# Performance work log

Measured on AMD Instinct MI355X. Metric: run time of the kernel, lower is better.

The kernel has to match this reference:

```python
import jax, jax.numpy as jnp
import numpy as np

HIDDEN = 768
INTER = 1536
N_EXPERTS = 8
TOP_K = 2
AUX_COEF = 0.01


def setup_inputs() -> dict:
    key = jax.random.key(0)
    k0, k1, k2, k3, k4 = jax.random.split(key, 5)
    B, S = 2, 1024
    x = jax.random.normal(k0, (B, S, HIDDEN), dtype=jnp.float32)
    # nn.Linear weights (no bias); stored pre-transposed for einsum (in, out)
    router_w = jax.random.normal(k1, (HIDDEN, N_EXPERTS), dtype=jnp.float32) * 0.02
    w_gate = jax.random.normal(k2, (N_EXPERTS, HIDDEN, INTER), dtype=jnp.float32) * 0.02
    w_up = jax.random.normal(k3, (N_EXPERTS, HIDDEN, INTER), dtype=jnp.float32) * 0.02
    w_down = jax.random.normal(k4, (N_EXPERTS, INTER, HIDDEN), dtype=jnp.float32) * 0.02
    return {"x": x, "router_w": router_w, "w_gate": w_gate, "w_up": w_up, "w_down": w_down}


def reference(x, router_w, w_gate, w_up, w_down):
    B, S, H = x.shape
    xf = x.reshape(-1, H)                      # [T, H]
    T = xf.shape[0]

    router_logits = xf @ router_w              # [T, E]
    router_probs = jax.nn.softmax(router_logits.astype(jnp.float32), axis=-1)
    topk_probs, topk_idx = jax.lax.top_k(router_probs, TOP_K)   # [T, K]
    topk_probs = topk_probs / topk_probs.sum(axis=-1, keepdims=True)

    # dense combine weights: [T, E]; top_k indices are distinct per token so add == set
    comb = jnp.zeros((T, N_EXPERTS), jnp.float32).at[
        jnp.arange(T)[:, None], topk_idx
    ].add(topk_probs)

    # SwiGLU for all experts (dense faithful form of the per-expert gather loop)
    g = jnp.einsum("th,ehi->tei", xf, w_gate)  # [T, E, I]
    u = jnp.einsum("th,ehi->tei", xf, w_up)
    expert_out = jnp.einsum("tei,eih->teh", jax.nn.silu(g) * u, w_down)  # [T, E, H]
    out = jnp.einsum("teh,te->th", expert_out, comb.astype(expert_out.dtype))

    # load-balancing aux loss
    tokens_per_expert = jnp.zeros(N_EXPERTS, jnp.float32).at[topk_idx.reshape(-1)].add(1.0)
    tokens_per_expert = tokens_per_expert / (T * TOP_K)
    router_prob_per_expert = router_probs.mean(axis=0)
    aux_loss = N_EXPERTS * (tokens_per_expert * router_prob_per_expert).sum() * AUX_COEF

    return out.reshape(B, S, H), aux_loss
```

## Files before the change

### kernel.cpp

```cpp
#include <hip/hip_runtime.h>
#include <math.h>


typedef unsigned short u16;
typedef __attribute__((ext_vector_type(8))) short bhalf8;
typedef __attribute__((ext_vector_type(4))) float floatx4;

#define HD 768
#define ID 1536
#define NE 8
#define TT 2048
#define SLOTS 5120
#define MT 40
#define RBLK 512

__device__ __forceinline__ float b2f(u16 u) {
    union { unsigned int i; float f; } v; v.i = ((unsigned int)u) << 16; return v.f;
}
__device__ __forceinline__ u16 f2b(float f) {
    union { float f; unsigned int i; } v; v.f = f;
    unsigned int i = v.i;
    return (u16)((i + 0x7FFFu + ((i >> 16) & 1u)) >> 16);
}
__device__ __forceinline__ void glds16(const u16* g, u16* l) {
    __builtin_amdgcn_global_load_lds(
        (const __attribute__((address_space(1))) unsigned int*)g,
        (__attribute__((address_space(3))) unsigned int*)l, 16, 0, 0);
}

__global__ void init_k(const u16* __restrict__ x16, int* flag,
                       int* hdr, int* tokof, float* pslot) {
    int i = blockIdx.x * 256 + threadIdx.x;
    if (i < 40) hdr[i] = 0;
    if (i < SLOTS) { tokof[i] = -1; pslot[i] = 0.f; }
    if (blockIdx.x == 0 && threadIdx.x >= 64 && threadIdx.x < 128) {
        int lane = threadIdx.x - 64, c = 0;
#pragma unroll
        for (int j = 0; j < 4; ++j) {
            u16 w = x16[lane + 64 * j];
            int ex = (w >> 7) & 0xFF;
            c += (ex >= 118 && ex <= 135);
        }
#pragma unroll
        for (int off = 32; off > 0; off >>= 1) c += __shfl_xor(c, off);
        if (lane == 0) *flag = (c >= 200) ? 1 : 0;
    }
}

__global__ void router_k(const void* __restrict__ x, const void* __restrict__ rw,
                         const int* __restrict__ flag,
                         int* topki, float* topkp, float* blockpart) {
    __shared__ float sp[4][NE];
    int lane = threadIdx.x & 63, wave = threadIdx.x >> 6;
    int t = blockIdx.x * 4 + wave;
    int bf = *flag;
    const float* xf = (const float*)x + (size_t)t * HD;
    const u16*   xh = (const u16*)x + (size_t)t * HD;
    const float* rf = (const float*)rw;
    const u16*   rh = (const u16*)rw;
    float acc[NE];
#pragma unroll
    for (int e = 0; e < NE; ++e) acc[e] = 0.f;
    for (int j = 0; j < HD / 64; ++j) {
        int h = lane + 64 * j;
        float xv = bf ? b2f(xh[h]) : xf[h];
#pragma unroll
        for (int e = 0; e < NE; ++e)
            acc[e] += xv * (bf ? b2f(rh[h * NE + e]) : rf[h * NE + e]);
    }
#pragma unroll
    for (int e = 0; e < NE; ++e) {
        float v = acc[e];
#pragma unroll
        for (int off = 32; off > 0; off >>= 1) v += __shfl_xor(v, off);
        acc[e] = v;
    }
    if (lane == 0) {
        float m = acc[0];
        for (int e = 1; e < NE; ++e) m = fmaxf(m, acc[e]);
        float p[NE], s = 0.f;
        for (int e = 0; e < NE; ++e) { p[e] = expf(acc[e] - m); s += p[e]; }
        float inv = 1.f / s;
        for (int e = 0; e < NE; ++e) { p[e] *= inv; sp[wave][e] = p[e]; }
        int i1 = 0; float p1 = p[0];
        for (int e = 1; e < NE; ++e) if (p[e] > p1) { p1 = p[e]; i1 = e; }
        int i2 = -1; float p2 = -1.f;
        for (int e = 0; e < NE; ++e) if (e != i1 && p[e] > p2) { p2 = p[e]; i2 = e; }
        if (i2 < 0) { i2 = (i1 + 1) & 7; p2 = p[i2]; }
        float sn = 1.f / (p1 + p2);
        topki[2 * t] = i1;  topki[2 * t + 1] = i2;
        topkp[2 * t] = p1 * sn;  topkp[2 * t + 1] = p2 * sn;
    }
    __syncthreads();
    if (threadIdx.x < NE)
        blockpart[blockIdx.x * NE + threadIdx.x] =
            sp[0][threadIdx.x] + sp[1][threadIdx.x] +
            sp[2][threadIdx.x] + sp[3][threadIdx.x];
}

__global__ void prefix_k(const int* __restrict__ topki,
                         const float* __restrict__ blockpart, int* base,
                         int* total, int* cursor, void* out, const int* flag) {
    __shared__ int hist[NE];
    __shared__ float psum[NE];
    int tid = threadIdx.x;
    if (tid < NE) { hist[tid] = 0; psum[tid] = 0.f; }
    __syncthreads();
    for (int i = tid; i < TT * 2; i += 256) atomicAdd(&hist[topki[i] & 7], 1);
    for (int i = tid; i < RBLK * NE; i += 256) atomicAdd(&psum[i & 7], blockpart[i]);
    __syncthreads();
    if (tid == 0) {
        int cum = 0; float aux = 0.f;
        for (int e = 0; e < NE; ++e) {
            int c = hist[e];
            base[e] = cum; cum += (c + 127) & ~127;
            cursor[e] = 0;
            aux += ((float)c / (float)(TT * 2)) * (psum[e] / (float)TT);
        }
        *total = cum;
        float auxv = aux * (float)NE * 0.01f;
        if (*flag) ((u16*)out)[(size_t)TT * HD] = f2b(auxv);
        else       ((float*)out)[(size_t)TT * HD] = auxv;
    }
}

__global__ void scatter_k(const int* __restrict__ topki, const float* __restrict__ topkp,
                          const int* __restrict__ base, int* cursor,
                          int* tokof, float* pslot, int* slotmap) {
    __shared__ int lcnt[NE], lbase[NE];
    int tid = threadIdx.x;
    int t = blockIdx.x * 256 + tid;
    if (tid < NE) lcnt[tid] = 0;
    __syncthreads();
    int e0 = topki[2 * t] & 7, e1 = topki[2 * t + 1] & 7;
    float q0 = topkp[2 * t], q1 = topkp[2 * t + 1];
    int l0 = atomicAdd(&lcnt[e0], 1);
    int l1 = atomicAdd(&lcnt[e1], 1);
    __syncthreads();
    if (tid < NE) lbase[tid] = atomicAdd(&cursor[tid], lcnt[tid]);
    __syncthreads();
    int s0 = min(max(base[e0] + lbase[e0] + l0, 0), SLOTS - 1);
    int s1 = min(max(base[e1] + lbase[e1] + l1, 0), SLOTS - 1);
    tokof[s0] = t;  pslot[s0] = q0;  slotmap[2 * t] = s0;
    tokof[s1] = t;  pslot[s1] = q1;  slotmap[2 * t + 1] = s1;
}

__global__ void apack_k(const void* __restrict__ x, const int* __restrict__ flag,
                        const int* __restrict__ tokof, const int* __restrict__ total,
                        u16* __restrict__ apack) {
    int mt = blockIdx.y, kt = blockIdx.x;
    if (mt * 128 >= *total) return;
    int tid = threadIdx.x;
    int ml = tid >> 1, half = tid & 1;
    int tok = tokof[mt * 128 + ml];
    union { uint4 v[4]; u16 u[32]; } buf;
    if ((unsigned)tok < (unsigned)TT) {
        if (*flag) {
            const u16* s = (const u16*)x + (size_t)tok * HD + kt * 64 + half * 32;
#pragma unroll
            for (int c = 0; c < 4; ++c) buf.v[c] = *(const uint4*)&s[c * 8];
        } else {
            const float* s = (const float*)x + (size_t)tok * HD + kt * 64 + half * 32;
#pragma unroll
            for (int c = 0; c < 8; ++c) {
                float4 f = *(const float4*)&s[c * 4];
                buf.u[c * 4 + 0] = f2b(f.x); buf.u[c * 4 + 1] = f2b(f.y);
                buf.u[c * 4 + 2] = f2b(f.z); buf.u[c * 4 + 3] = f2b(f.w);
            }
        }
    } else {
#pragma unroll
        for (int c = 0; c < 4; ++c) buf.v[c] = make_uint4(0, 0, 0, 0);
    }
    u16* dst = apack + (((size_t)mt * 12 + kt) << 13) + ml * 64;
#pragma unroll
    for (int c = 0; c < 4; ++c) {
        int pc = (half * 4 + c) ^ (ml & 7);
        *(uint4*)(dst + pc * 8) = buf.v[c];
    }
}

__global__ void wpack_k(const void* __restrict__ srcA, const void* __restrict__ srcB,
                        u16* __restrict__ dstA, u16* __restrict__ dstB,
                        int K, int N, int ktiles, int ntiles,
                        const int* __restrict__ flag) {
    __shared__ u16 t[8192];
    int z = blockIdx.z;
    const void* src = (srcB != nullptr && z >= NE) ? srcB : srcA;
    u16* dst = (dstB != nullptr && z >= NE) ? dstB : dstA;
    int e = z & 7;
    int kt = blockIdx.x, nt = blockIdx.y;
    int tid = threadIdx.x;
    int kr = tid >> 2, ng = (tid & 3) * 32;
    size_t srow = ((size_t)e * K + (size_t)kt * 64 + kr) * N + (size_t)nt * 128 + ng;
    union { uint4 v[4]; u16 u[32]; } buf;
    if (*flag) {
        const u16* s = (const u16*)src + srow;
#pragma unroll
        for (int c = 0; c < 4; ++c) buf.v[c] = *(const uint4*)&s[c * 8];
    } else {
        const float* s = (const float*)src + srow;
#pragma unroll
        for (int c = 0; c < 8; ++c) {
            float4 f = *(const float4*)&s[c * 4];
            buf.u[c * 4 + 0] = f2b(f.x); buf.u[c * 4 + 1] = f2b(f.y);
            buf.u[c * 4 + 2] = f2b(f.z); buf.u[c * 4 + 3] = f2b(f.w);
        }
    }
#pragma unroll
    for (int jj = 0; jj < 32; ++jj) {
        int n = ng + jj;
        t[n * 64 + (((kr >> 3) ^ (n & 7)) << 3) + (kr & 7)] = buf.u[jj];
    }
    __syncthreads();
    u16* d = dst + ((((size_t)e * ntiles + nt) * ktiles + kt) << 13);
#pragma unroll
    for (int i = 0; i < 4; ++i) {
        int off = tid * 8 + i * 2048;
        *(uint4*)(d + off) = *(const uint4*)&t[off];
    }
}

__global__ __launch_bounds__(256, 2) void gemm1_k(
        const u16* __restrict__ apack, const u16* __restrict__ wgp,
        const u16* __restrict__ wup, const int* __restrict__ base,
        const int* __restrict__ total, u16* __restrict__ actp) {
    __shared__ u16 smem[24576];
    u16* As = smem; u16* Bg = smem + 8192; u16* Bu = smem + 16384;
    int mt = blockIdx.y;
    if (mt * 128 >= *total) return;
    int e = 7;
    while (e > 0 && mt * 128 < base[e]) --e;
    int nt = blockIdx.x;
    int tid = threadIdx.x, lane = tid & 63, wave = tid >> 6;
    int wm = (wave & 1) * 64, wn = (wave >> 1) * 64;
    int llo = lane & 15, lq = lane >> 4;
    const u16* atile = apack + (((size_t)mt * 12) << 13);
    const u16* gtile = wgp + ((((size_t)e * 12 + nt) * 12) << 13);
    const u16* utile = wup + ((((size_t)e * 12 + nt) * 12) << 13);
    floatx4 accG[4][4], accU[4][4];
#pragma unroll
    for (int i = 0; i < 4; ++i)
#pragma unroll
        for (int j = 0; j < 4; ++j) {
            accG[i][j] = floatx4{0.f, 0.f, 0.f, 0.f};
            accU[i][j] = floatx4{0.f, 0.f, 0.f, 0.f};
        }
    for (int kt = 0; kt < 12; ++kt) {
        const u16* ga = atile + (kt << 13);
        const u16* gg = gtile + (kt << 13);
        const u16* gu = utile + (kt << 13);
        __syncthreads();
#pragma unroll
        for (int i = 0; i < 4; ++i) {
            int off = tid * 8 + i * 2048;
            glds16(ga + off, As + off);
            glds16(gg + off, Bg + off);
            glds16(gu + off, Bu + off);
        }
        asm volatile("s_waitcnt vmcnt(0)" ::: "memory");
        __syncthreads();
#pragma unroll
        for (int kk = 0; kk < 2; ++kk) {
            int q = kk * 4 + lq;
            bhalf8 af[4], bg[4], bu[4];
#pragma unroll
            for (int i = 0; i < 4; ++i) {
                int m = wm + i * 16 + llo;
                af[i] = *(const bhalf8*)&As[m * 64 + ((q ^ (m & 7)) << 3)];
                int n = wn + i * 16 + llo;
                bg[i] = *(const bhalf8*)&Bg[n * 64 + ((q ^ (n & 7)) << 3)];
                bu[i] = *(const bhalf8*)&Bu[n * 64 + ((q ^ (n & 7)) << 3)];
            }
#pragma unroll
            for (int i = 0; i < 4; ++i)
#pragma unroll
                for (int j = 0; j < 4; ++j) {
                    accG[i][j] = __builtin_amdgcn_mfma_f32_16x16x32_bf16(af[i], bg[j], accG[i][j], 0, 0, 0);
                    accU[i][j] = __builtin_amdgcn_mfma_f32_16x16x32_bf16(af[i], bu[j], accU[i][j], 0, 0, 0);
                }
        }
    }
    __syncthreads();
    u16* Ah = smem;
    int q4 = lq * 4;
#pragma unroll
    for (int i = 0; i < 4; ++i)
#pragma unroll
        for (int j = 0; j < 4; ++j)
#pragma unroll
            for (int rr = 0; rr < 4; ++rr) {
                int m = wm + i * 16 + q4 + rr;
                int n = wn + j * 16 + llo;
                float g = accG[i][j][rr], u = accU[i][j][rr];
                Ah[m * 128 + n] = f2b((g / (1.f + expf(-g))) * u);
            }
    __syncthreads();
    u16* dst = actp + (((size_t)mt * 24 + nt * 2) << 13);
#pragma unroll
    for (int s = 0; s < 2; ++s)
#pragma unroll
        for (int i = 0; i < 4; ++i) {
            int off = tid * 8 + i * 2048;
            int m = off >> 6;
            int pc = (off >> 3) & 7;
            int q = pc ^ (m & 7);
            *(uint4*)(dst + ((size_t)s << 13) + off) =
                *(const uint4*)&Ah[m * 128 + s * 64 + q * 8];
        }
}

__global__ __launch_bounds__(256, 2) void gemm2_k(
        const u16* __restrict__ actp, const u16* __restrict__ wdp,
        const int* __restrict__ base, const int* __restrict__ total,
        const float* __restrict__ pslot, float* __restrict__ y) {
    __shared__ u16 smem[16384];
    u16* As = smem; u16* Bs = smem + 8192;
    int mt = blockIdx.y;
    if (mt * 128 >= *total) return;
    int e = 7;
    while (e > 0 && mt * 128 < base[e]) --e;
    int nt = blockIdx.x;
    int tid = threadIdx.x, lane = tid & 63, wave = tid >> 6;
    int wm = (wave & 1) * 64, wn = (wave >> 1) * 64;
    int llo = lane & 15, lq = lane >> 4;
    const u16* atile = actp + (((size_t)mt * 24) << 13);
    const u16* btile = wdp + ((((size_t)e * 6 + nt) * 24) << 13);
    floatx4 acc[4][4];
#pragma unroll
    for (int i = 0; i < 4; ++i)
#pragma unroll
        for (int j = 0; j < 4; ++j) acc[i][j] = floatx4{0.f, 0.f, 0.f, 0.f};
    for (int kt = 0; kt < 24; ++kt) {
        const u16* ga = atile + (kt << 13);
        const u16* gb = btile + (kt << 13);
        __syncthreads();
#pragma unroll
        for (int i = 0; i < 4; ++i) {
            int off = tid * 8 + i * 2048;
            glds16(ga + off, As + off);
            glds16(gb + off, Bs + off);
        }
        asm volatile("s_waitcnt vmcnt(0)" ::: "memory");
        __syncthreads();
#pragma unroll
        for (int kk = 0; kk < 2; ++kk) {
            int q = kk * 4 + lq;
            bhalf8 af[4], bf[4];
#pragma unroll
            for (int i = 0; i < 4; ++i) {
                int m = wm + i * 16 + llo;
                af[i] = *(const bhalf8*)&As[m * 64 + ((q ^ (m & 7)) << 3)];
                int n = wn + i * 16 + llo;
                bf[i] = *(const bhalf8*)&Bs[n * 64 + ((q ^ (n & 7)) << 3)];
            }
#pragma unroll
            for (int i = 0; i < 4; ++i)
#pragma unroll
                for (int j = 0; j < 4; ++j)
                    acc[i][j] = __builtin_amdgcn_mfma_f32_16x16x32_bf16(af[i], bf[j], acc[i][j], 0, 0, 0);
        }
    }
    int q4 = lq * 4;
#pragma unroll
    for (int i = 0; i < 4; ++i)
#pragma unroll
        for (int rr = 0; rr < 4; ++rr) {
            int m = mt * 128 + wm + i * 16 + q4 + rr;
            float p = pslot[m];
#pragma unroll
            for (int j = 0; j < 4; ++j) {
                int n = nt * 128 + wn + j * 16 + llo;
                y[(size_t)m * HD + n] = p * acc[i][j][rr];
            }
        }
}

__global__ void combine_k(const float* __restrict__ y, const int* __restrict__ slotmap,
                          void* __restrict__ out, const int* __restrict__ flag) {
    int g = blockIdx.x * 256 + threadIdx.x;
    int t = g / 192;
    int q = (g % 192) * 4;
    int s0 = min(max(slotmap[2 * t], 0), SLOTS - 1);
    int s1 = min(max(slotmap[2 * t + 1], 0), SLOTS - 1);
    float4 a = *(const float4*)&y[(size_t)s0 * HD + q];
    float4 b = *(const float4*)&y[(size_t)s1 * HD + q];
    float4 rv;
    rv.x = a.x + b.x; rv.y = a.y + b.y; rv.z = a.z + b.z; rv.w = a.w + b.w;
    if (*flag) {
        ushort4 o;
        o.x = f2b(rv.x); o.y = f2b(rv.y); o.z = f2b(rv.z); o.w = f2b(rv.w);
        *(ushort4*)((u16*)out + (size_t)t * HD + q) = o;
    } else {
        *(float4*)((float*)out + (size_t)t * HD + q) = rv;
    }
}

extern "C" void kernel_launch(void* const* d_in, const int* in_sizes, int n_in,
                              void* d_out, int out_size, void* d_ws, size_t ws_size,
                              hipStream_t stream) {
    const void* x  = d_in[0];
    const void* rw = d_in[1];
    const void* wg = d_in[2];
    const void* wu = d_in[3];
    const void* wd = d_in[4];
    char* ws = (char*)d_ws;

    int*   hdr     = (int*)(ws + 0);
    int*   cursor  = (int*)(ws + 32);
    int*   base    = (int*)(ws + 64);
    int*   total   = (int*)(ws + 96);
    int*   flag    = (int*)(ws + 224);
    int*   topki   = (int*)(ws + 256);
    float* topkp   = (float*)(ws + 16640);
    int*   tokof   = (int*)(ws + 33024);
    float* pslot   = (float*)(ws + 53504);
    int*   slotmap = (int*)(ws + 73984);
    float* blockpart = (float*)(ws + 90368);
    u16*   apack   = (u16*)(ws + 106752);
    u16*   actp    = (u16*)(ws + 7971072);
    u16*   wgp     = (u16*)(ws + 23699712);
    u16*   wup     = (u16*)(ws + 42574080);
    u16*   wdp     = (u16*)(ws + 61448448);
    float* ybuf    = (float*)(ws + 23699712);
    if (ws_size < 80322816u) return;

    init_k<<<20, 256, 0, stream>>>((const u16*)x, flag, hdr, tokof, pslot);
    router_k<<<RBLK, 256, 0, stream>>>(x, rw, flag, topki, topkp, blockpart);
    prefix_k<<<1, 256, 0, stream>>>(topki, blockpart, base, total, cursor, d_out, flag);
    scatter_k<<<TT / 256, 256, 0, stream>>>(topki, topkp, base, cursor,
                                            tokof, pslot, slotmap);
    apack_k<<<dim3(12, MT), 256, 0, stream>>>(x, flag, tokof, total, apack);
    wpack_k<<<dim3(12, 12, 16), 256, 0, stream>>>(wg, wu, wgp, wup,
                                                  HD, ID, 12, 12, flag);
    wpack_k<<<dim3(24, 6, 8), 256, 0, stream>>>(wd, nullptr, wdp, nullptr,
                                                ID, HD, 24, 6, flag);
    gemm1_k<<<dim3(12, MT), 256, 0, stream>>>(apack, wgp, wup, base, total, actp);
    gemm2_k<<<dim3(6, MT), 256, 0, stream>>>(actp, wdp, base, total, pslot, ybuf);
    combine_k<<<(TT * 192) / 256, 256, 0, stream>>>(ybuf, slotmap, d_out, flag);
}
```

Measured before the change: 266.8 us.

## Fuse MoE pipeline into one persistent kernel with grid-wide barriers

```diff
diff --git a/kernel.cpp b/kernel.cpp
--- a/kernel.cpp
+++ b/kernel.cpp
@@ -11,8 +11,7 @@
 #define NE 8
 #define TT 2048
 #define SLOTS 5120
-#define MT 40
-#define RBLK 512
+#define NBLK 256
 
 __device__ __forceinline__ float b2f(u16 u) {
     union { unsigned int i; float f; } v; v.i = ((unsigned int)u) << 16; return v.f;
@@ -28,173 +27,35 @@
         (__attribute__((address_space(3))) unsigned int*)l, 16, 0, 0);
 }
 
-__global__ void init_k(const u16* __restrict__ x16, int* flag,
-                       int* hdr, int* tokof, float* pslot) {
-    int i = blockIdx.x * 256 + threadIdx.x;
-    if (i < 40) hdr[i] = 0;
-    if (i < SLOTS) { tokof[i] = -1; pslot[i] = 0.f; }
-    if (blockIdx.x == 0 && threadIdx.x >= 64 && threadIdx.x < 128) {
-        int lane = threadIdx.x - 64, c = 0;
-#pragma unroll
-        for (int j = 0; j < 4; ++j) {
-            u16 w = x16[lane + 64 * j];
-            int ex = (w >> 7) & 0xFF;
-            c += (ex >= 118 && ex <= 135);
-        }
-#pragma unroll
-        for (int off = 32; off > 0; off >>= 1) c += __shfl_xor(c, off);
-        if (lane == 0) *flag = (c >= 200) ? 1 : 0;
-    }
-}
-
-__global__ void router_k(const void* __restrict__ x, const void* __restrict__ rw,
-                         const int* __restrict__ flag,
-                         int* topki, float* topkp, float* blockpart) {
-    __shared__ float sp[4][NE];
-    int lane = threadIdx.x & 63, wave = threadIdx.x >> 6;
-    int t = blockIdx.x * 4 + wave;
-    int bf = *flag;
-    const float* xf = (const float*)x + (size_t)t * HD;
-    const u16*   xh = (const u16*)x + (size_t)t * HD;
-    const float* rf = (const float*)rw;
-    const u16*   rh = (const u16*)rw;
-    float acc[NE];
-#pragma unroll
-    for (int e = 0; e < NE; ++e) acc[e] = 0.f;
-    for (int j = 0; j < HD / 64; ++j) {
-        int h = lane + 64 * j;
-        float xv = bf ? b2f(xh[h]) : xf[h];
-#pragma unroll
-        for (int e = 0; e < NE; ++e)
-            acc[e] += xv * (bf ? b2f(rh[h * NE + e]) : rf[h * NE + e]);
-    }
-#pragma unroll
-    for (int e = 0; e < NE; ++e) {
-        float v = acc[e];
-#pragma unroll
-        for (int off = 32; off > 0; off >>= 1) v += __shfl_xor(v, off);
-        acc[e] = v;
-    }
-    if (lane == 0) {
-        float m = acc[0];
-        for (int e = 1; e < NE; ++e) m = fmaxf(m, acc[e]);
-        float p[NE], s = 0.f;
-        for (int e = 0; e < NE; ++e) { p[e] = expf(acc[e] - m); s += p[e]; }
-        float inv = 1.f / s;
-        for (int e = 0; e < NE; ++e) { p[e] *= inv; sp[wave][e] = p[e]; }
-        int i1 = 0; float p1 = p[0];
-        for (int e = 1; e < NE; ++e) if (p[e] > p1) { p1 = p[e]; i1 = e; }
-        int i2 = -1; float p2 = -1.f;
-        for (int e = 0; e < NE; ++e) if (e != i1 && p[e] > p2) { p2 = p[e]; i2 = e; }
-        if (i2 < 0) { i2 = (i1 + 1) & 7; p2 = p[i2]; }
-        float sn = 1.f / (p1 + p2);
-        topki[2 * t] = i1;  topki[2 * t + 1] = i2;
-        topkp[2 * t] = p1 * sn;  topkp[2 * t + 1] = p2 * sn;
-    }
+__device__ __forceinline__ void gbar(int* cnt, int* gen) {
     __syncthreads();
-    if (threadIdx.x < NE)
-        blockpart[blockIdx.x * NE + threadIdx.x] =
-            sp[0][threadIdx.x] + sp[1][threadIdx.x] +
-            sp[2][threadIdx.x] + sp[3][threadIdx.x];
-}
-
-__global__ void prefix_k(const int* __restrict__ topki,
-                         const float* __restrict__ blockpart, int* base,
-                         int* total, int* cursor, void* out, const int* flag) {
-    __shared__ int hist[NE];
-    __shared__ float psum[NE];
-    int tid = threadIdx.x;
-    if (tid < NE) { hist[tid] = 0; psum[tid] = 0.f; }
+    if (threadIdx.x == 0) {
+        __threadfence();
+        int g = __hip_atomic_load(gen, __ATOMIC_RELAXED, __HIP_MEMORY_SCOPE_AGENT);
+        int a = __hip_atomic_fetch_add(cnt, 1, __ATOMIC_ACQ_REL, __HIP_MEMORY_SCOPE_AGENT);
+        if (a == NBLK - 1) {
+            __hip_atomic_store(cnt, 0, __ATOMIC_RELAXED, __HIP_MEMORY_SCOPE_AGENT);
+            __hip_atomic_store(gen, g + 1, __ATOMIC_RELEASE, __HIP_MEMORY_SCOPE_AGENT);
+        } else {
+            while (__hip_atomic_load(gen, __ATOMIC_ACQUIRE, __HIP_MEMORY_SCOPE_AGENT) == g)
+                __builtin_amdgcn_s_sleep(8);
+        }
+        __threadfence();
+    }
     __syncthreads();
-    for (int i = tid; i < TT * 2; i += 256) atomicAdd(&hist[topki[i] & 7], 1);
-    for (int i = tid; i < RBLK * NE; i += 256) atomicAdd(&psum[i & 7], blockpart[i]);
-    __syncthreads();
-    if (tid == 0) {
-        int cum = 0; float aux = 0.f;
-        for (int e = 0; e < NE; ++e) {
-            int c = hist[e];
-            base[e] = cum; cum += (c + 127) & ~127;
-            cursor[e] = 0;
-            aux += ((float)c / (float)(TT * 2)) * (psum[e] / (float)TT);
-        }
-        *total = cum;
-        float auxv = aux * (float)NE * 0.01f;
-        if (*flag) ((u16*)out)[(size_t)TT * HD] = f2b(auxv);
-        else       ((float*)out)[(size_t)TT * HD] = auxv;
-    }
-}
-
-__global__ void scatter_k(const int* __restrict__ topki, const float* __restrict__ topkp,
-                          const int* __restrict__ base, int* cursor,
-                          int* tokof, float* pslot, int* slotmap) {
-    __shared__ int lcnt[NE], lbase[NE];
-    int tid = threadIdx.x;
-    int t = blockIdx.x * 256 + tid;
-    if (tid < NE) lcnt[tid] = 0;
-    __syncthreads();
-    int e0 = topki[2 * t] & 7, e1 = topki[2 * t + 1] & 7;
-    float q0 = topkp[2 * t], q1 = topkp[2 * t + 1];
-    int l0 = atomicAdd(&lcnt[e0], 1);
-    int l1 = atomicAdd(&lcnt[e1], 1);
-    __syncthreads();
-    if (tid < NE) lbase[tid] = atomicAdd(&cursor[tid], lcnt[tid]);
-    __syncthreads();
-    int s0 = min(max(base[e0] + lbase[e0] + l0, 0), SLOTS - 1);
-    int s1 = min(max(base[e1] + lbase[e1] + l1, 0), SLOTS - 1);
-    tokof[s0] = t;  pslot[s0] = q0;  slotmap[2 * t] = s0;
-    tokof[s1] = t;  pslot[s1] = q1;  slotmap[2 * t + 1] = s1;
-}
-
-__global__ void apack_k(const void* __restrict__ x, const int* __restrict__ flag,
-                        const int* __restrict__ tokof, const int* __restrict__ total,
-                        u16* __restrict__ apack) {
-    int mt = blockIdx.y, kt = blockIdx.x;
-    if (mt * 128 >= *total) return;
-    int tid = threadIdx.x;
-    int ml = tid >> 1, half = tid & 1;
-    int tok = tokof[mt * 128 + ml];
-    union { uint4 v[4]; u16 u[32]; } buf;
-    if ((unsigned)tok < (unsigned)TT) {
-        if (*flag) {
-            const u16* s = (const u16*)x + (size_t)tok * HD + kt * 64 + half * 32;
-#pragma unroll
-            for (int c = 0; c < 4; ++c) buf.v[c] = *(const uint4*)&s[c * 8];
-        } else {
-            const float* s = (const float*)x + (size_t)tok * HD + kt * 64 + half * 32;
-#pragma unroll
-            for (int c = 0; c < 8; ++c) {
-                float4 f = *(const float4*)&s[c * 4];
-                buf.u[c * 4 + 0] = f2b(f.x); buf.u[c * 4 + 1] = f2b(f.y);
-                buf.u[c * 4 + 2] = f2b(f.z); buf.u[c * 4 + 3] = f2b(f.w);
-            }
-        }
-    } else {
-#pragma unroll
-        for (int c = 0; c < 4; ++c) buf.v[c] = make_uint4(0, 0, 0, 0);
-    }
-    u16* dst = apack + (((size_t)mt * 12 + kt) << 13) + ml * 64;
-#pragma unroll
-    for (int c = 0; c < 4; ++c) {
-        int pc = (half * 4 + c) ^ (ml & 7);
-        *(uint4*)(dst + pc * 8) = buf.v[c];
-    }
-}
-
-__global__ void wpack_k(const void* __restrict__ srcA, const void* __restrict__ srcB,
-                        u16* __restrict__ dstA, u16* __restrict__ dstB,
-                        int K, int N, int ktiles, int ntiles,
-                        const int* __restrict__ flag) {
-    __shared__ u16 t[8192];
-    int z = blockIdx.z;
-    const void* src = (srcB != nullptr && z >= NE) ? srcB : srcA;
-    u16* dst = (dstB != nullptr && z >= NE) ? dstB : dstA;
-    int e = z & 7;
-    int kt = blockIdx.x, nt = blockIdx.y;
-    int tid = threadIdx.x;
+}
+
+__global__ void init_k(char* ws) {
+    if (threadIdx.x < 64) ((int*)ws)[threadIdx.x] = 0;
+}
+
+__device__ __forceinline__ void wpack_body(
+        const void* __restrict__ src, u16* __restrict__ dst, int K, int N,
+        int ktiles, int ntiles, int e, int kt, int nt, int bf, u16* t, int tid) {
     int kr = tid >> 2, ng = (tid & 3) * 32;
     size_t srow = ((size_t)e * K + (size_t)kt * 64 + kr) * N + (size_t)nt * 128 + ng;
     union { uint4 v[4]; u16 u[32]; } buf;
-    if (*flag) {
+    if (bf) {
         const u16* s = (const u16*)src + srow;
 #pragma unroll
         for (int c = 0; c < 4; ++c) buf.v[c] = *(const uint4*)&s[c * 8];
@@ -221,200 +82,24 @@
     }
 }
 
-__global__ __launch_bounds__(256, 2) void gemm1_k(
-        const u16* __restrict__ apack, const u16* __restrict__ wgp,
-        const u16* __restrict__ wup, const int* __restrict__ base,
-        const int* __restrict__ total, u16* __restrict__ actp) {
+__global__ __launch_bounds__(256, 1) void moe_mega(
+        const void* __restrict__ x, const void* __restrict__ rw,
+        const void* __restrict__ wg, const void* __restrict__ wu,
+        const void* __restrict__ wd, void* __restrict__ out,
+        char* __restrict__ ws) {
     __shared__ u16 smem[24576];
-    u16* As = smem; u16* Bg = smem + 8192; u16* Bu = smem + 16384;
-    int mt = blockIdx.y;
-    if (mt * 128 >= *total) return;
-    int e = 7;
-    while (e > 0 && mt * 128 < base[e]) --e;
-    int nt = blockIdx.x;
-    int tid = threadIdx.x, lane = tid & 63, wave = tid >> 6;
-    int wm = (wave & 1) * 64, wn = (wave >> 1) * 64;
-    int llo = lane & 15, lq = lane >> 4;
-    const u16* atile = apack + (((size_t)mt * 12) << 13);
-    const u16* gtile = wgp + ((((size_t)e * 12 + nt) * 12) << 13);
-    const u16* utile = wup + ((((size_t)e * 12 + nt) * 12) << 13);
-    floatx4 accG[4][4], accU[4][4];
-#pragma unroll
-    for (int i = 0; i < 4; ++i)
-#pragma unroll
-        for (int j = 0; j < 4; ++j) {
-            accG[i][j] = floatx4{0.f, 0.f, 0.f, 0.f};
-            accU[i][j] = floatx4{0.f, 0.f, 0.f, 0.f};
-        }
-    for (int kt = 0; kt < 12; ++kt) {
-        const u16* ga = atile + (kt << 13);
-        const u16* gg = gtile + (kt << 13);
-        const u16* gu = utile + (kt << 13);
-        __syncthreads();
-#pragma unroll
-        for (int i = 0; i < 4; ++i) {
-            int off = tid * 8 + i * 2048;
-            glds16(ga + off, As + off);
-            glds16(gg + off, Bg + off);
-            glds16(gu + off, Bu + off);
-        }
-        asm volatile("s_waitcnt vmcnt(0)" ::: "memory");
-        __syncthreads();
-#pragma unroll
-        for (int kk = 0; kk < 2; ++kk) {
-            int q = kk * 4 + lq;
-            bhalf8 af[4], bg[4], bu[4];
-#pragma unroll
-            for (int i = 0; i < 4; ++i) {
-                int m = wm + i * 16 + llo;
-                af[i] = *(const bhalf8*)&As[m * 64 + ((q ^ (m & 7)) << 3)];
-                int n = wn + i * 16 + llo;
-                bg[i] = *(const bhalf8*)&Bg[n * 64 + ((q ^ (n & 7)) << 3)];
-                bu[i] = *(const bhalf8*)&Bu[n * 64 + ((q ^ (n & 7)) << 3)];
-            }
-#pragma unroll
-            for (int i = 0; i < 4; ++i)
-#pragma unroll
-                for (int j = 0; j < 4; ++j) {
-                    accG[i][j] = __builtin_amdgcn_mfma_f32_16x16x32_bf16(af[i], bg[j], accG[i][j], 0, 0, 0);
-                    accU[i][j] = __builtin_amdgcn_mfma_f32_16x16x32_bf16(af[i], bu[j], accU[i][j], 0, 0, 0);
-                }
-        }
-    }
-    __syncthreads();
-    u16* Ah = smem;
-    int q4 = lq * 4;
-#pragma unroll
-    for (int i = 0; i < 4; ++i)
-#pragma unroll
-        for (int j = 0; j < 4; ++j)
-#pragma unroll
-            for (int rr = 0; rr < 4; ++rr) {
-                int m = wm + i * 16 + q4 + rr;
-                int n = wn + j * 16 + llo;
-                float g = accG[i][j][rr], u = accU[i][j][rr];
-                Ah[m * 128 + n] = f2b((g / (1.f + expf(-g))) * u);
-            }
-    __syncthreads();
-    u16* dst = actp + (((size_t)mt * 24 + nt * 2) << 13);
-#pragma unroll
-    for (int s = 0; s < 2; ++s)
-#pragma unroll
-        for (int i = 0; i < 4; ++i) {
-            int off = tid * 8 + i * 2048;
-            int m = off >> 6;
-            int pc = (off >> 3) & 7;
-            int q = pc ^ (m & 7);
-            *(uint4*)(dst + ((size_t)s << 13) + off) =
-                *(const uint4*)&Ah[m * 128 + s * 64 + q * 8];
-        }
-}
-
-__global__ __launch_bounds__(256, 2) void gemm2_k(
-        const u16* __restrict__ actp, const u16* __restrict__ wdp,
-        const int* __restrict__ base, const int* __restrict__ total,
-        const float* __restrict__ pslot, float* __restrict__ y) {
-    __shared__ u16 smem[16384];
-    u16* As = smem; u16* Bs = smem + 8192;
-    int mt = blockIdx.y;
-    if (mt * 128 >= *total) return;
-    int e = 7;
-    while (e > 0 && mt * 128 < base[e]) --e;
-    int nt = blockIdx.x;
-    int tid = threadIdx.x, lane = tid & 63, wave = tid >> 6;
-    int wm = (wave & 1) * 64, wn = (wave >> 1) * 64;
-    int llo = lane & 15, lq = lane >> 4;
-    const u16* atile = actp + (((size_t)mt * 24) << 13);
-    const u16* btile = wdp + ((((size_t)e * 6 + nt) * 24) << 13);
-    floatx4 acc[4][4];
-#pragma unroll
-    for (int i = 0; i < 4; ++i)
-#pragma unroll
-        for (int j = 0; j < 4; ++j) acc[i][j] = floatx4{0.f, 0.f, 0.f, 0.f};
-    for (int kt = 0; kt < 24; ++kt) {
-        const u16* ga = atile + (kt << 13);
-        const u16* gb = btile + (kt << 13);
-        __syncthreads();
-#pragma unroll
-        for (int i = 0; i < 4; ++i) {
-            int off = tid * 8 + i * 2048;
-            glds16(ga + off, As + off);
-            glds16(gb + off, Bs + off);
-        }
-        asm volatile("s_waitcnt vmcnt(0)" ::: "memory");
-        __syncthreads();
-#pragma unroll
-        for (int kk = 0; kk < 2; ++kk) {
-            int q = kk * 4 + lq;
-            bhalf8 af[4], bf[4];
-#pragma unroll
-            for (int i = 0; i < 4; ++i) {
-                int m = wm + i * 16 + llo;
-                af[i] = *(const bhalf8*)&As[m * 64 + ((q ^ (m & 7)) << 3)];
-                int n = wn + i * 16 + llo;
-                bf[i] = *(const bhalf8*)&Bs[n * 64 + ((q ^ (n & 7)) << 3)];
-            }
-#pragma unroll
-            for (int i = 0; i < 4; ++i)
-#pragma unroll
-                for (int j = 0; j < 4; ++j)
-                    acc[i][j] = __builtin_amdgcn_mfma_f32_16x16x32_bf16(af[i], bf[j], acc[i][j], 0, 0, 0);
-        }
-    }
-    int q4 = lq * 4;
-#pragma unroll
-    for (int i = 0; i < 4; ++i)
-#pragma unroll
-        for (int rr = 0; rr < 4; ++rr) {
-            int m = mt * 128 + wm + i * 16 + q4 + rr;
-            float p = pslot[m];
-#pragma unroll
-            for (int j = 0; j < 4; ++j) {
-                int n = nt * 128 + wn + j * 16 + llo;
-                y[(size_t)m * HD + n] = p * acc[i][j][rr];
-            }
-        }
-}
-
-__global__ void combine_k(const float* __restrict__ y, const int* __restrict__ slotmap,
-                          void* __restrict__ out, const int* __restrict__ flag) {
-    int g = blockIdx.x * 256 + threadIdx.x;
-    int t = g / 192;
-    int q = (g % 192) * 4;
-    int s0 = min(max(slotmap[2 * t], 0), SLOTS - 1);
-    int s1 = min(max(slotmap[2 * t + 1], 0), SLOTS - 1);
-    float4 a = *(const float4*)&y[(size_t)s0 * HD + q];
-    float4 b = *(const float4*)&y[(size_t)s1 * HD + q];
-    float4 rv;
-    rv.x = a.x + b.x; rv.y = a.y + b.y; rv.z = a.z + b.z; rv.w = a.w + b.w;
-    if (*flag) {
-        ushort4 o;
-        o.x = f2b(rv.x); o.y = f2b(rv.y); o.z = f2b(rv.z); o.w = f2b(rv.w);
-        *(ushort4*)((u16*)out + (size_t)t * HD + q) = o;
-    } else {
-        *(float4*)((float*)out + (size_t)t * HD + q) = rv;
-    }
-}
-
-extern "C" void kernel_launch(void* const* d_in, const int* in_sizes, int n_in,
-                              void* d_out, int out_size, void* d_ws, size_t ws_size,
-                              hipStream_t stream) {
-    const void* x  = d_in[0];
-    const void* rw = d_in[1];
-    const void* wg = d_in[2];
-    const void* wu = d_in[3];
-    const void* wd = d_in[4];
-    char* ws = (char*)d_ws;
-
-    int*   hdr     = (int*)(ws + 0);
-    int*   cursor  = (int*)(ws + 32);
-    int*   base    = (int*)(ws + 64);
-    int*   total   = (int*)(ws + 96);
-    int*   flag    = (int*)(ws + 224);
+    const int bid = blockIdx.x, tid = threadIdx.x;
+    const int lane = tid & 63, wave = tid >> 6;
+
+    int*   cursorp = (int*)(ws + 32);
+    int*   basep   = (int*)(ws + 64);
+    int*   totalp  = (int*)(ws + 96);
+    int*   bcnt    = (int*)(ws + 128);
+    int*   bgen    = (int*)(ws + 160);
     int*   topki   = (int*)(ws + 256);
     float* topkp   = (float*)(ws + 16640);
     int*   tokof   = (int*)(ws + 33024);
-    float* pslot   = (float*)(ws + 53504);
+    float* pslotp  = (float*)(ws + 53504);
     int*   slotmap = (int*)(ws + 73984);
     float* blockpart = (float*)(ws + 90368);
     u16*   apack   = (u16*)(ws + 106752);
@@ -423,19 +108,359 @@
     u16*   wup     = (u16*)(ws + 42574080);
     u16*   wdp     = (u16*)(ws + 61448448);
     float* ybuf    = (float*)(ws + 23699712);
+
+    int bf;
+    {
+        if (tid < 64) {
+            int c = 0;
+#pragma unroll
+            for (int j = 0; j < 4; ++j) {
+                u16 w = ((const u16*)x)[tid + 64 * j];
+                int ex = (w >> 7) & 0xFF;
+                c += (ex >= 118 && ex <= 135);
+            }
+#pragma unroll
+            for (int off = 32; off > 0; off >>= 1) c += __shfl_xor(c, off);
+            if (tid == 0) *(int*)smem = (c >= 200) ? 1 : 0;
+        }
+        __syncthreads();
+        bf = *(int*)smem;
+        __syncthreads();
+    }
+
+    for (int i = bid * 256 + tid; i < SLOTS; i += NBLK * 256) {
+        tokof[i] = -1; pslotp[i] = 0.f;
+    }
+    for (int rep = 0; rep < 2; ++rep) {
+        float* sp = (float*)smem;
+        int t = (rep * NBLK + bid) * 4 + wave;
+        const float* xf = (const float*)x + (size_t)t * HD;
+        const u16*   xh = (const u16*)x + (size_t)t * HD;
+        const float* rf = (const float*)rw;
+        const u16*   rh = (const u16*)rw;
+        float acc[NE];
+#pragma unroll
+        for (int e = 0; e < NE; ++e) acc[e] = 0.f;
+        for (int j = 0; j < HD / 64; ++j) {
+            int h = lane + 64 * j;
+            float xv = bf ? b2f(xh[h]) : xf[h];
+#pragma unroll
+            for (int e = 0; e < NE; ++e)
+                acc[e] += xv * (bf ? b2f(rh[h * NE + e]) : rf[h * NE + e]);
+        }
+#pragma unroll
+        for (int e = 0; e < NE; ++e) {
+            float v = acc[e];
+#pragma unroll
+            for (int off = 32; off > 0; off >>= 1) v += __shfl_xor(v, off);
+            acc[e] = v;
+        }
+        if (lane == 0) {
+            float m = acc[0];
+            for (int e = 1; e < NE; ++e) m = fmaxf(m, acc[e]);
+            float p[NE], s = 0.f;
+            for (int e = 0; e < NE; ++e) { p[e] = expf(acc[e] - m); s += p[e]; }
+            float inv = 1.f / s;
+            for (int e = 0; e < NE; ++e) { p[e] *= inv; sp[wave * NE + e] = p[e]; }
+            int i1 = 0; float p1 = p[0];
+            for (int e = 1; e < NE; ++e) if (p[e] > p1) { p1 = p[e]; i1 = e; }
+            int i2 = -1; float p2 = -1.f;
+            for (int e = 0; e < NE; ++e) if (e != i1 && p[e] > p2) { p2 = p[e]; i2 = e; }
+            if (i2 < 0) { i2 = (i1 + 1) & 7; p2 = p[i2]; }
+            float sn = 1.f / (p1 + p2);
+            topki[2 * t] = i1;  topki[2 * t + 1] = i2;
+            topkp[2 * t] = p1 * sn;  topkp[2 * t + 1] = p2 * sn;
+        }
+        __syncthreads();
+        if (tid < NE)
+            blockpart[(rep * NBLK + bid) * NE + tid] =
+                sp[tid] + sp[NE + tid] + sp[2 * NE + tid] + sp[3 * NE + tid];
+        __syncthreads();
+    }
+    for (int T = bid; T < 3456; T += NBLK) {
+        const void* src; u16* dst; int K, N, ktiles, ntiles, e, kt, nt;
+        if (T < 2304) {
+            int z = T / 144, rem = T - z * 144;
+            nt = rem / 12; kt = rem - nt * 12;
+            e = z & 7;
+            src = (z < NE) ? wg : wu;
+            dst = (z < NE) ? wgp : wup;
+            K = HD; N = ID; ktiles = 12; ntiles = 12;
+        } else {
+            int T2 = T - 2304;
+            e = T2 / 144; int rem = T2 - e * 144;
+            nt = rem / 24; kt = rem - nt * 24;
+            src = wd; dst = wdp; K = ID; N = HD; ktiles = 24; ntiles = 6;
+        }
+        wpack_body(src, dst, K, N, ktiles, ntiles, e, kt, nt, bf, smem, tid);
+        __syncthreads();
+    }
+    gbar(bcnt, bgen);
+
+    if (bid == 0) {
+        int* hist = (int*)smem;
+        float* psum = (float*)((char*)smem + 64);
+        if (tid < NE) { hist[tid] = 0; psum[tid] = 0.f; }
+        __syncthreads();
+        for (int i = tid; i < TT * 2; i += 256) atomicAdd(&hist[topki[i] & 7], 1);
+        for (int i = tid; i < 512 * NE; i += 256) atomicAdd(&psum[i & 7], blockpart[i]);
+        __syncthreads();
+        if (tid == 0) {
+            int cum = 0; float aux = 0.f;
+            for (int e = 0; e < NE; ++e) {
+                int c = hist[e];
+                basep[e] = cum; cum += (c + 127) & ~127;
+                cursorp[e] = 0;
+                aux += ((float)c / (float)(TT * 2)) * (psum[e] / (float)TT);
+            }
+            *totalp = cum;
+            float auxv = aux * (float)NE * 0.01f;
+            if (bf) ((u16*)out)[(size_t)TT * HD] = f2b(auxv);
+            else    ((float*)out)[(size_t)TT * HD] = auxv;
+        }
+    }
+    gbar(bcnt, bgen);
+
+    if (bid < 8) {
+        int* lcnt = (int*)smem;
+        int* lbase = (int*)((char*)smem + 64);
+        if (tid < NE) lcnt[tid] = 0;
+        __syncthreads();
+        int t = bid * 256 + tid;
+        int e0 = topki[2 * t] & 7, e1 = topki[2 * t + 1] & 7;
+        float q0 = topkp[2 * t], q1 = topkp[2 * t + 1];
+        int l0 = atomicAdd(&lcnt[e0], 1);
+        int l1 = atomicAdd(&lcnt[e1], 1);
+        __syncthreads();
+        if (tid < NE) lbase[tid] = atomicAdd(&cursorp[tid], lcnt[tid]);
+        __syncthreads();
+        int s0 = min(max(basep[e0] + lbase[e0] + l0, 0), SLOTS - 1);
+        int s1 = min(max(basep[e1] + lbase[e1] + l1, 0), SLOTS - 1);
+        tokof[s0] = t;  pslotp[s0] = q0;  slotmap[2 * t] = s0;
+        tokof[s1] = t;  pslotp[s1] = q1;  slotmap[2 * t + 1] = s1;
+    }
+    gbar(bcnt, bgen);
+
+    {
+        int total = *totalp;
+        for (int T = bid; T < 480; T += NBLK) {
+            int mt = T / 12, kt = T - mt * 12;
+            if (mt * 128 >= total) continue;
+            int ml = tid >> 1, half = tid & 1;
+            int tok = tokof[mt * 128 + ml];
+            union { uint4 v[4]; u16 u[32]; } buf;
+            if ((unsigned)tok < (unsigned)TT) {
+                if (bf) {
+                    const u16* s = (const u16*)x + (size_t)tok * HD + kt * 64 + half * 32;
+#pragma unroll
+                    for (int c = 0; c < 4; ++c) buf.v[c] = *(const uint4*)&s[c * 8];
+                } else {
+                    const float* s = (const float*)x + (size_t)tok * HD + kt * 64 + half * 32;
+#pragma unroll
+                    for (int c = 0; c < 8; ++c) {
+                        float4 f = *(const float4*)&s[c * 4];
+                        buf.u[c * 4 + 0] = f2b(f.x); buf.u[c * 4 + 1] = f2b(f.y);
+                        buf.u[c * 4 + 2] = f2b(f.z); buf.u[c * 4 + 3] = f2b(f.w);
+                    }
+                }
+            } else {
+#pragma unroll
+                for (int c = 0; c < 4; ++c) buf.v[c] = make_uint4(0, 0, 0, 0);
+            }
+            u16* dst = apack + (((size_t)mt * 12 + kt) << 13) + ml * 64;
+#pragma unroll
+            for (int c = 0; c < 4; ++c) {
+                int pc = (half * 4 + c) ^ (ml & 7);
+                *(uint4*)(dst + pc * 8) = buf.v[c];
+            }
+        }
+    }
+    gbar(bcnt, bgen);
+
+    {
+        int total = *totalp;
+        for (int T = bid; T < 480; T += NBLK) {
+            int mt = T / 12, nt = T - mt * 12;
+            if (mt * 128 >= total) continue;
+            u16* As = smem; u16* Bg = smem + 8192; u16* Bu = smem + 16384;
+            int e = 7;
+            while (e > 0 && mt * 128 < basep[e]) --e;
+            int wm = (wave & 1) * 64, wn = (wave >> 1) * 64;
+            int llo = lane & 15, lq = lane >> 4;
+            const u16* atile = apack + (((size_t)mt * 12) << 13);
+            const u16* gtile = wgp + ((((size_t)e * 12 + nt) * 12) << 13);
+            const u16* utile = wup + ((((size_t)e * 12 + nt) * 12) << 13);
+            floatx4 accG[4][4], accU[4][4];
+#pragma unroll
+            for (int i = 0; i < 4; ++i)
+#pragma unroll
+                for (int j = 0; j < 4; ++j) {
+                    accG[i][j] = floatx4{0.f, 0.f, 0.f, 0.f};
+                    accU[i][j] = floatx4{0.f, 0.f, 0.f, 0.f};
+                }
+            for (int kt = 0; kt < 12; ++kt) {
+                const u16* ga = atile + (kt << 13);
+                const u16* gg = gtile + (kt << 13);
+                const u16* gu = utile + (kt << 13);
+                __syncthreads();
+#pragma unroll
+                for (int i = 0; i < 4; ++i) {
+                    int off = tid * 8 + i * 2048;
+                    glds16(ga + off, As + off);
+                    glds16(gg + off, Bg + off);
+                    glds16(gu + off, Bu + off);
+                }
+                asm volatile("s_waitcnt vmcnt(0)" ::: "memory");
+                __syncthreads();
+#pragma unroll
+                for (int kk = 0; kk < 2; ++kk) {
+                    int q = kk * 4 + lq;
+                    bhalf8 af[4], bg[4], bu[4];
+#pragma unroll
+                    for (int i = 0; i < 4; ++i) {
+                        int m = wm + i * 16 + llo;
+                        af[i] = *(const bhalf8*)&As[m * 64 + ((q ^ (m & 7)) << 3)];
+                        int n = wn + i * 16 + llo;
+                        bg[i] = *(const bhalf8*)&Bg[n * 64 + ((q ^ (n & 7)) << 3)];
+                        bu[i] = *(const bhalf8*)&Bu[n * 64 + ((q ^ (n & 7)) << 3)];
+                    }
+#pragma unroll
+                    for (int i = 0; i < 4; ++i)
+#pragma unroll
+                        for (int j = 0; j < 4; ++j) {
+                            accG[i][j] = __builtin_amdgcn_mfma_f32_16x16x32_bf16(af[i], bg[j], accG[i][j], 0, 0, 0);
+                            accU[i][j] = __builtin_amdgcn_mfma_f32_16x16x32_bf16(af[i], bu[j], accU[i][j], 0, 0, 0);
+                        }
+                }
+            }
+            __syncthreads();
+            u16* Ah = smem;
+            int q4 = lq * 4;
+#pragma unroll
+            for (int i = 0; i < 4; ++i)
+#pragma unroll
+                for (int j = 0; j < 4; ++j)
+#pragma unroll
+                    for (int rr = 0; rr < 4; ++rr) {
+                        int m = wm + i * 16 + q4 + rr;
+                        int n = wn + j * 16 + llo;
+                        float g = accG[i][j][rr], u = accU[i][j][rr];
+                        Ah[m * 128 + n] = f2b((g / (1.f + expf(-g))) * u);
+                    }
+            __syncthreads();
+            u16* dst = actp + (((size_t)mt * 24 + nt * 2) << 13);
+#pragma unroll
+            for (int s = 0; s < 2; ++s)
+#pragma unroll
+                for (int i = 0; i < 4; ++i) {
+                    int off = tid * 8 + i * 2048;
+                    int m = off >> 6;
+                    int pc = (off >> 3) & 7;
+                    int q = pc ^ (m & 7);
+                    *(uint4*)(dst + ((size_t)s << 13) + off) =
+                        *(const uint4*)&Ah[m * 128 + s * 64 + q * 8];
+                }
+            __syncthreads();
+        }
+    }
+    gbar(bcnt, bgen);
+
+    {
+        int total = *totalp;
+        for (int T = bid; T < 240; T += NBLK) {
+            int mt = T / 6, nt = T - mt * 6;
+            if (mt * 128 >= total) continue;
+            u16* As = smem; u16* Bs = smem + 8192;
+            int e = 7;
+            while (e > 0 && mt * 128 < basep[e]) --e;
+            int wm = (wave & 1) * 64, wn = (wave >> 1) * 64;
+            int llo = lane & 15, lq = lane >> 4;
+            const u16* atile = actp + (((size_t)mt * 24) << 13);
+            const u16* btile = wdp + ((((size_t)e * 6 + nt) * 24) << 13);
+            floatx4 acc[4][4];
+#pragma unroll
+            for (int i = 0; i < 4; ++i)
+#pragma unroll
+                for (int j = 0; j < 4; ++j) acc[i][j] = floatx4{0.f, 0.f, 0.f, 0.f};
+            for (int kt = 0; kt < 24; ++kt) {
+                const u16* ga = atile + (kt << 13);
+                const u16* gb = btile + (kt << 13);
+                __syncthreads();
+#pragma unroll
+                for (int i = 0; i < 4; ++i) {
+                    int off = tid * 8 + i * 2048;
+                    glds16(ga + off, As + off);
+                    glds16(gb + off, Bs + off);
+                }
+                asm volatile("s_waitcnt vmcnt(0)" ::: "memory");
+                __syncthreads();
+#pragma unroll
+                for (int kk = 0; kk < 2; ++kk) {
+                    int q = kk * 4 + lq;
+                    bhalf8 af[4], bfr[4];
+#pragma unroll
+                    for (int i = 0; i < 4; ++i) {
+                        int m = wm + i * 16 + llo;
+                        af[i] = *(const bhalf8*)&As[m * 64 + ((q ^ (m & 7)) << 3)];
+                        int n = wn + i * 16 + llo;
+                        bfr[i] = *(const bhalf8*)&Bs[n * 64 + ((q ^ (n & 7)) << 3)];
+                    }
+#pragma unroll
+                    for (int i = 0; i < 4; ++i)
+#pragma unroll
+                        for (int j = 0; j < 4; ++j)
+                            acc[i][j] = __builtin_amdgcn_mfma_f32_16x16x32_bf16(af[i], bfr[j], acc[i][j], 0, 0, 0);
+                }
+            }
+            int q4 = lq * 4;
+#pragma unroll
+            for (int i = 0; i < 4; ++i)
+#pragma unroll
+                for (int rr = 0; rr < 4; ++rr) {
+                    int m = mt * 128 + wm + i * 16 + q4 + rr;
+                    float p = pslotp[m];
+#pragma unroll
+                    for (int j = 0; j < 4; ++j) {
+                        int n = nt * 128 + wn + j * 16 + llo;
+                        ybuf[(size_t)m * HD + n] = p * acc[i][j][rr];
+                    }
+                }
+            __syncthreads();
+        }
+    }
+    gbar(bcnt, bgen);
+
+#pragma unroll
+    for (int r = 0; r < 6; ++r) {
+        int g = (r * NBLK + bid) * 256 + tid;
+        int t = g / 192;
+        int q = (g - t * 192) * 4;
+        int s0 = min(max(slotmap[2 * t], 0), SLOTS - 1);
+        int s1 = min(max(slotmap[2 * t + 1], 0), SLOTS - 1);
+        float4 a = *(const float4*)&ybuf[(size_t)s0 * HD + q];
+        float4 b = *(const float4*)&ybuf[(size_t)s1 * HD + q];
+        float4 rv;
+        rv.x = a.x + b.x; rv.y = a.y + b.y; rv.z = a.z + b.z; rv.w = a.w + b.w;
+        if (bf) {
+            ushort4 o;
+            o.x = f2b(rv.x); o.y = f2b(rv.y); o.z = f2b(rv.z); o.w = f2b(rv.w);
+            *(ushort4*)((u16*)out + (size_t)t * HD + q) = o;
+        } else {
+            *(float4*)((float*)out + (size_t)t * HD + q) = rv;
+        }
+    }
+}
+
+extern "C" void kernel_launch(void* const* d_in, const int* in_sizes, int n_in,
+                              void* d_out, int out_size, void* d_ws, size_t ws_size,
+                              hipStream_t stream) {
     if (ws_size < 80322816u) return;
-
-    init_k<<<20, 256, 0, stream>>>((const u16*)x, flag, hdr, tokof, pslot);
-    router_k<<<RBLK, 256, 0, stream>>>(x, rw, flag, topki, topkp, blockpart);
-    prefix_k<<<1, 256, 0, stream>>>(topki, blockpart, base, total, cursor, d_out, flag);
-    scatter_k<<<TT / 256, 256, 0, stream>>>(topki, topkp, base, cursor,
-                                            tokof, pslot, slotmap);
-    apack_k<<<dim3(12, MT), 256, 0, stream>>>(x, flag, tokof, total, apack);
-    wpack_k<<<dim3(12, 12, 16), 256, 0, stream>>>(wg, wu, wgp, wup,
-                                                  HD, ID, 12, 12, flag);
-    wpack_k<<<dim3(24, 6, 8), 256, 0, stream>>>(wd, nullptr, wdp, nullptr,
-                                                ID, HD, 24, 6, flag);
-    gemm1_k<<<dim3(12, MT), 256, 0, stream>>>(apack, wgp, wup, base, total, actp);
-    gemm2_k<<<dim3(6, MT), 256, 0, stream>>>(actp, wdp, base, total, pslot, ybuf);
-    combine_k<<<(TT * 192) / 256, 256, 0, stream>>>(ybuf, slotmap, d_out, flag);
-}
+    const void* x  = d_in[0];
+    const void* rw = d_in[1];
+    const void* wg = d_in[2];
+    const void* wu = d_in[3];
+    const void* wd = d_in[4];
+    char* ws = (char*)d_ws;
+    init_k<<<1, 64, 0, stream>>>(ws);
+    moe_mega<<<NBLK, 256, 0, stream>>>(x, rw, wg, wu, wd, d_out, ws);
+}
```

Result: slower. 575.6 us (+115.7%).
